# Kernel optimization log

Measured on AMD Instinct MI355X. Metric: run time of the kernel, lower is better.

## Reference

```python
import jax, jax.numpy as jnp
import numpy as np

N = 100000
E = 1600000
IN, HID, OUT = 128, 256, 64


def _glorot(key, fan_in, fan_out):
    s = 1.0 / np.sqrt(fan_in)
    return jax.random.uniform(key, (fan_in, fan_out), jnp.float32, -s, s)


def setup_inputs() -> dict:
    key = jax.random.key(0)
    ks = jax.random.split(key, 12)
    x = jax.random.normal(ks[0], (N, IN), jnp.float32)
    edge_index = jax.random.randint(ks[1], (2, E), 0, N, jnp.int64)
    dims = [(IN, HID), (HID, HID), (HID, OUT), (OUT, OUT)]
    inp = {"x": x, "edge_index": edge_index}
    for i, (fi, fo) in enumerate(dims, start=1):
        inp[f"Wl{i}"] = _glorot(ks[2 * i], fi, fo)        # aggregated-neighbor weight (lin_l)
        inp[f"Wr{i}"] = _glorot(ks[2 * i + 1], fi, fo)    # root/self weight (lin_r)
        inp[f"b{i}"] = jnp.zeros((fo,), jnp.float32)
    return inp


def _sage_conv(x, src, dst, Wl, Wr, b):
    # mean aggregation of source features into destination nodes
    msg_sum = jax.ops.segment_sum(x[src], dst, num_segments=N)           # [N, d_in]
    cnt = jax.ops.segment_sum(jnp.ones((src.shape[0],), x.dtype), dst, num_segments=N)
    mean = msg_sum / jnp.maximum(cnt, 1.0)[:, None]
    return mean @ Wl + x @ Wr + b


def reference(x, edge_index, Wl1, Wr1, b1, Wl2, Wr2, b2, Wl3, Wr3, b3, Wl4, Wr4, b4):
    src, dst = edge_index[0], edge_index[1]
    # conv1 = GraphSAGE(in, hid, num_layers=2): SAGEConv->ReLU->SAGEConv
    h = jax.nn.relu(_sage_conv(x, src, dst, Wl1, Wr1, b1))
    h = _sage_conv(h, src, dst, Wl2, Wr2, b2)
    # model-level ReLU between conv1 and conv2
    h = jax.nn.relu(h)
    # conv2 = GraphSAGE(hid, out, num_layers=2)
    h = jax.nn.relu(_sage_conv(h, src, dst, Wl3, Wr3, b3))
    h = _sage_conv(h, src, dst, Wl4, Wr4, b4)
    return jax.nn.log_softmax(h, axis=1)
```

## Files before the change

### kernel.cpp

```cpp
#include <hip/hip_runtime.h>
#include <cstdint>
#include <cstddef>


typedef short s16x8 __attribute__((ext_vector_type(8)));
typedef float f32x4 __attribute__((ext_vector_type(4)));
typedef float f32x2 __attribute__((ext_vector_type(2)));
typedef unsigned short u16;
typedef unsigned short u16x8 __attribute__((ext_vector_type(8)));
typedef unsigned char u8;
typedef unsigned char u8x8 __attribute__((ext_vector_type(8)));

#define EPB 8192
#define EPT 32
#define GCAP 6144

#if __has_builtin(__builtin_amdgcn_cvt_pk_f32_fp8) && __has_builtin(__builtin_amdgcn_cvt_pk_fp8_f32)
#define HWFP8 1
#else
#define HWFP8 0
#endif

__device__ __forceinline__ float b2f(u16 u) {
    union { unsigned int i; float f; } x; x.i = ((unsigned int)u) << 16; return x.f;
}
__device__ __forceinline__ u16 f2b(float f) {
    union { float f; unsigned int i; } x; x.f = f;
    unsigned int r = x.i + 0x7FFFu + ((x.i >> 16) & 1u);
    return (u16)(r >> 16);
}

#if !HWFP8
__device__ __forceinline__ u8 f2q_sw(float f) {
    union { float f; unsigned int i; } x; x.f = f;
    unsigned s = (x.i >> 24) & 0x80u;
    unsigned a = x.i & 0x7FFFFFFFu;
    a += 0x7FFFFu + ((a >> 20) & 1u);
    if (a < 0x3C800000u) return (u8)s;
    if (a > 0x43EFFFFFu) a = 0x43E00000u;
    unsigned e = (a >> 23) - 120u;
    unsigned m = (a >> 20) & 7u;
    return (u8)(s | (e << 3) | m);
}
__device__ __forceinline__ float q2f_sw(u8 u) {
    unsigned v = u & 0x7Fu;
    if (v == 0) return 0.f;
    union { unsigned int i; float f; } x;
    x.i = ((unsigned)(u & 0x80u) << 24) | (((v >> 3) + 120u) << 23) | ((v & 7u) << 20);
    return x.f;
}
#endif

__device__ __forceinline__ void dec8(u8x8 v, float* o) {
#if HWFP8
    union { u8x8 b; unsigned int d[2]; } u; u.b = v;
    f32x2 p;
    p = __builtin_amdgcn_cvt_pk_f32_fp8(u.d[0], false); o[0] = p[0]; o[1] = p[1];
    p = __builtin_amdgcn_cvt_pk_f32_fp8(u.d[0], true);  o[2] = p[0]; o[3] = p[1];
    p = __builtin_amdgcn_cvt_pk_f32_fp8(u.d[1], false); o[4] = p[0]; o[5] = p[1];
    p = __builtin_amdgcn_cvt_pk_f32_fp8(u.d[1], true);  o[6] = p[0]; o[7] = p[1];
#else
#pragma unroll
    for (int j = 0; j < 8; ++j) o[j] = q2f_sw(v[j]);
#endif
}
__device__ __forceinline__ u8x8 enc8(const float* f) {
#if HWFP8
    union { unsigned int d[2]; u8x8 b; } u;
    int d0 = __builtin_amdgcn_cvt_pk_fp8_f32(f[0], f[1], 0, false);
    d0 = __builtin_amdgcn_cvt_pk_fp8_f32(f[2], f[3], d0, true);
    int d1 = __builtin_amdgcn_cvt_pk_fp8_f32(f[4], f[5], 0, false);
    d1 = __builtin_amdgcn_cvt_pk_fp8_f32(f[6], f[7], d1, true);
    u.d[0] = (unsigned)d0; u.d[1] = (unsigned)d1;
    return u.b;
#else
    u8x8 q;
#pragma unroll
    for (int j = 0; j < 8; ++j) q[j] = f2q_sw(f[j]);
    return q;
#endif
}
__device__ __forceinline__ u8 enc1(float v) {
#if HWFP8
    return (u8)(__builtin_amdgcn_cvt_pk_fp8_f32(v, v, 0, false) & 0xFF);
#else
    return f2q_sw(v);
#endif
}


__global__ __launch_bounds__(256) void bucket_pass1(
    const int* __restrict__ src, const int* __restrict__ dst, int E,
    unsigned* __restrict__ gOffs, unsigned* __restrict__ staged, int nbkt)
{
    __shared__ unsigned offs[1025];
    __shared__ unsigned tsum[256];
    const int tid = threadIdx.x;
    const int e0 = blockIdx.x * EPB;

    for (int i = tid; i < nbkt; i += 256) offs[i] = 0u;
    __syncthreads();

    for (int t = 0; t < EPT; ++t) {
        int e = e0 + t * 256 + tid;
        if (e < E) atomicAdd(&offs[((unsigned)dst[e]) >> 7], 1u);
    }
    __syncthreads();

    unsigned c[4], sum = 0;
#pragma unroll
    for (int i = 0; i < 4; ++i) {
        int idx = tid * 4 + i;
        c[i] = sum;
        sum += (idx < nbkt) ? offs[idx] : 0u;
    }
    tsum[tid] = sum;
    __syncthreads();
    for (int off = 1; off < 256; off <<= 1) {
        unsigned v = (tid >= off) ? tsum[tid - off] : 0u;
        __syncthreads();
        tsum[tid] += v;
        __syncthreads();
    }
    unsigned base = (tid == 0) ? 0u : tsum[tid - 1];
    unsigned total = tsum[255];
#pragma unroll
    for (int i = 0; i < 4; ++i) {
        int idx = tid * 4 + i;
        if (idx < nbkt) offs[idx] = base + c[i];
    }
    if (tid == 0) offs[nbkt] = total;
    __syncthreads();

    for (int i = tid; i <= nbkt; i += 256)
        gOffs[(size_t)blockIdx.x * (nbkt + 1) + i] = offs[i];
    __syncthreads();

    for (int t = 0; t < EPT; ++t) {
        int e = e0 + t * 256 + tid;
        if (e < E) {
            unsigned d = (unsigned)dst[e];
            unsigned s = (unsigned)src[e];
            unsigned p = atomicAdd(&offs[d >> 7], 1u);
            staged[(size_t)e0 + p] = (s << 7) | (d & 127u);
        }
    }
}


__global__ void colsum_kernel(const unsigned* __restrict__ gOffs, int nblk, int nbkt,
                              unsigned* __restrict__ bktCnt) {
    int b = blockIdx.x * 256 + threadIdx.x;
    if (b >= nbkt) return;
    unsigned s = 0;
    for (int blk = 0; blk < nblk; ++blk) {
        const unsigned* row = gOffs + (size_t)blk * (nbkt + 1);
        s += row[b + 1] - row[b];
    }
    bktCnt[b] = s;
}


__global__ __launch_bounds__(1024) void scan_base(
    const unsigned* __restrict__ bktCnt, int nbkt, unsigned* __restrict__ bktBase)
{
    __shared__ unsigned lds[1024];
    int t = threadIdx.x;
    unsigned v = (t < nbkt) ? bktCnt[t] : 0u;
    lds[t] = v;
    __syncthreads();
    for (int off = 1; off < 1024; off <<= 1) {
        unsigned u = (t >= off) ? lds[t - off] : 0u;
        __syncthreads();
        lds[t] += u;
        __syncthreads();
    }
    if (t <= nbkt) bktBase[t] = lds[t] - v;
}


__global__ __launch_bounds__(256) void bucket_gather(
    const unsigned* __restrict__ gOffs, const unsigned* __restrict__ staged,
    const unsigned* __restrict__ bktBase, int nblk, int nbkt, int Nn, int E,
    int* __restrict__ ssrc, int* __restrict__ rp)
{
    __shared__ unsigned segS[256];
    __shared__ unsigned segBase[257];
    __shared__ unsigned tsum[256];
    __shared__ unsigned nodeCnt[128];
    __shared__ unsigned cursor[128];
    __shared__ unsigned ents[GCAP];
    const int tid = threadIdx.x;
    const int bkt = blockIdx.x;
    const int stride = nbkt + 1;

    unsigned len = 0;
    if (tid < nblk) {
        unsigned s = gOffs[(size_t)tid * stride + bkt];
        unsigned e = gOffs[(size_t)tid * stride + bkt + 1];
        segS[tid] = s;
        len = e - s;
    }
    tsum[tid] = len;
    __syncthreads();
    for (int off = 1; off < 256; off <<= 1) {
        unsigned u = (tid >= off) ? tsum[tid - off] : 0u;
        __syncthreads();
        tsum[tid] += u;
        __syncthreads();
    }
    segBase[tid] = tsum[tid] - len;
    if (tid == 255) segBase[256] = tsum[255];
    if (tid < 128) nodeCnt[tid] = 0u;
    __syncthreads();

    const unsigned total = segBase[nblk];
    const bool cached = (total <= (unsigned)GCAP);

    if (cached) {
        const int grp = tid >> 4, l16 = tid & 15;
        for (int sg = grp; sg < nblk; sg += 16) {
            unsigned b0 = segBase[sg];
            unsigned slen = segBase[sg + 1] - b0;
            unsigned s0 = segS[sg];
            for (unsigned j = l16; j < slen; j += 16)
                ents[b0 + j] = staged[(size_t)sg * EPB + s0 + j];
        }
        __syncthreads();
        for (unsigned p = tid; p < total; p += 256)
            atomicAdd(&nodeCnt[ents[p] & 127u], 1u);
    } else {
        for (unsigned p = tid; p < total; p += 256) {
            int lo = 0, hi = nblk;
            while (hi - lo > 1) {
                int mid = (lo + hi) >> 1;
                if (segBase[mid] <= p) lo = mid; else hi = mid;
            }
            unsigned ent = staged[(size_t)lo * EPB + segS[lo] + (p - segBase[lo])];
            atomicAdd(&nodeCnt[ent & 127u], 1u);
        }
    }
    __syncthreads();

    unsigned nc = (tid < 128) ? nodeCnt[tid] : 0u;
    tsum[tid] = nc;
    __syncthreads();
    for (int off = 1; off < 128; off <<= 1) {
        unsigned u = (tid >= off) ? tsum[tid - off] : 0u;
        __syncthreads();
        tsum[tid] += u;
        __syncthreads();
    }
    if (tid < 128) {
        unsigned off0 = tsum[tid] - nc;
        cursor[tid] = off0;
        int node = bkt * 128 + tid;
        if (node < Nn) rp[node] = (int)(bktBase[bkt] + off0);
    }
    if (bkt == 0 && tid == 0) rp[Nn] = E;
    __syncthreads();

    const unsigned gbase = bktBase[bkt];
    if (cached) {
        for (unsigned p = tid; p < total; p += 256) {
            unsigned ent = ents[p];
            unsigned pos = atomicAdd(&cursor[ent & 127u], 1u);
            ssrc[gbase + pos] = (int)(ent >> 7);
        }
    } else {
        for (unsigned p = tid; p < total; p += 256) {
            int lo = 0, hi = nblk;
            while (hi - lo > 1) {
                int mid = (lo + hi) >> 1;
                if (segBase[mid] <= p) lo = mid; else hi = mid;
            }
            unsigned ent = staged[(size_t)lo * EPB + segS[lo] + (p - segBase[lo])];
            unsigned pos = atomicAdd(&cursor[ent & 127u], 1u);
            ssrc[gbase + pos] = (int)(ent >> 7);
        }
    }
}


__device__ __forceinline__ void wtr(const float* W, int K, int Nout, u16* Wt,
                                    int rowOff, int idx) {
    int k = idx / Nout, n = idx - k * Nout;
    Wt[(size_t)(n + rowOff) * K + k] = f2b(W[idx]);
}

__global__ void prep_all(
    const float* __restrict__ x, u16* __restrict__ xb, u8* __restrict__ x8,
    long xchunks,
    const float* __restrict__ Wl1, const float* __restrict__ Wr1,
    const float* __restrict__ Wl2, const float* __restrict__ Wr2,
    const float* __restrict__ Wl3, const float* __restrict__ Wr3,
    const float* __restrict__ Wl4, const float* __restrict__ Wr4,
    const float* __restrict__ b3, const float* __restrict__ b4,
    u16* __restrict__ W1lt, u16* __restrict__ W1rt,
    u16* __restrict__ W2lt, u16* __restrict__ W2rt,
    u16* __restrict__ W3t,  u16* __restrict__ W4t,
    float* __restrict__ b3c, float* __restrict__ b4c)
{
    long gidx = (long)blockIdx.x * 256 + threadIdx.x;
    if (gidx < xchunks) {
        long i = gidx * 8;
        float4 a = *(const float4*)(x + i);
        float4 b = *(const float4*)(x + i + 4);
        float f[8] = {a.x, a.y, a.z, a.w, b.x, b.y, b.z, b.w};
        u16x8 v;
#pragma unroll
        for (int j = 0; j < 8; ++j) v[j] = f2b(f[j]);
        *(u16x8*)(xb + i) = v;
        *(u8x8*)(x8 + i) = enc8(f);
        return;
    }
    int idx = (int)(gidx - xchunks);
    if (idx < 32768) { wtr(Wl1, 128, 256, W1lt, 0, idx); return; }
    idx -= 32768;
    if (idx < 32768) { wtr(Wr1, 128, 256, W1rt, 0, idx); return; }
    idx -= 32768;
    if (idx < 65536) { wtr(Wl2, 256, 256, W2lt, 0, idx); return; }
    idx -= 65536;
    if (idx < 65536) { wtr(Wr2, 256, 256, W2rt, 0, idx); return; }
    idx -= 65536;
    if (idx < 16384) { wtr(Wl3, 256, 64, W3t, 0, idx); return; }
    idx -= 16384;
    if (idx < 16384) { wtr(Wr3, 256, 64, W3t, 64, idx); return; }
    idx -= 16384;
    if (idx < 4096)  { wtr(Wl4, 64, 64, W4t, 0, idx); return; }
    idx -= 4096;
    if (idx < 4096)  { wtr(Wr4, 64, 64, W4t, 64, idx); return; }
    idx -= 4096;
    if (idx < 128)   { b3c[idx] = (idx < 64) ? 0.f : b3[idx - 64]; return; }
    idx -= 128;
    if (idx < 128)   { b4c[idx] = (idx < 64) ? 0.f : b4[idx - 64]; return; }
}


template <int LPN, bool ADD, bool RELU, bool LSM>
__global__ __launch_bounds__(256) void agg_kernel(
    const u8* __restrict__ feat, int ldF,
    const u16* __restrict__ addB, int ldA, int offA,
    void* __restrict__ outp, int ldO,
    const int* __restrict__ rp, const int* __restrict__ ssrc, int Nn)
{
    constexpr int NPW = 64 / LPN;
    int lane = threadIdx.x & 63;
    int wid  = threadIdx.x >> 6;
    int sub  = lane / LPN;
    int sl   = lane % LPN;
    int n = (blockIdx.x * 4 + wid) * NPW + sub;
    if (n >= Nn) return;

    int s = rp[n], e = rp[n + 1];
    float acc[8] = {0.f, 0.f, 0.f, 0.f, 0.f, 0.f, 0.f, 0.f};
    const u8* fbase = feat + (size_t)sl * 8;

    float t[8];
    for (int k = s; k < e; k += 8) {
        int last = e - 1;
        int sc[8];
#pragma unroll
        for (int i = 0; i < 8; ++i) {
            int ki = k + i;
            sc[i] = ssrc[ki <= last ? ki : last];
        }
        u8x8 v[8];
#pragma unroll
        for (int i = 0; i < 8; ++i)
            v[i] = *(const u8x8*)(fbase + (size_t)sc[i] * ldF);
#pragma unroll
        for (int i = 0; i < 8; ++i) {
            if (k + i < e) {
                dec8(v[i], t);
#pragma unroll
                for (int j = 0; j < 8; ++j) acc[j] += t[j];
            }
        }
    }

    int cnt = e - s;
    float inv = 1.0f / (float)(cnt > 0 ? cnt : 1);
#pragma unroll
    for (int j = 0; j < 8; ++j) acc[j] *= inv;

    if constexpr (ADD) {
        u16x8 v = *(const u16x8*)(addB + (size_t)n * ldA + offA + (size_t)sl * 8);
#pragma unroll
        for (int j = 0; j < 8; ++j) acc[j] += b2f(v[j]);
    }
    if constexpr (RELU) {
#pragma unroll
        for (int j = 0; j < 8; ++j) acc[j] = fmaxf(acc[j], 0.f);
    }

    if constexpr (LSM) {
        float m = acc[0];
#pragma unroll
        for (int j = 1; j < 8; ++j) m = fmaxf(m, acc[j]);
#pragma unroll
        for (int off = 1; off < 8; off <<= 1) m = fmaxf(m, __shfl_xor(m, off));
        float ss = 0.f;
#pragma unroll
        for (int j = 0; j < 8; ++j) ss += expf(acc[j] - m);
#pragma unroll
        for (int off = 1; off < 8; off <<= 1) ss += __shfl_xor(ss, off);
        float lse = m + logf(ss);
        float* o = (float*)outp + (size_t)n * ldO + (size_t)sl * 8;
        *(float4*)o = make_float4(acc[0] - lse, acc[1] - lse, acc[2] - lse, acc[3] - lse);
        *(float4*)(o + 4) = make_float4(acc[4] - lse, acc[5] - lse, acc[6] - lse, acc[7] - lse);
    } else {
        u16x8 v;
#pragma unroll
        for (int j = 0; j < 8; ++j) v[j] = f2b(acc[j]);
        *(u16x8*)((u16*)outp + (size_t)n * ldO + (size_t)sl * 8) = v;
    }
}


template <bool DUAL, bool RELU>
__global__ __launch_bounds__(512, 4) void gemm_mfma(
    const u16* __restrict__ A1, const u16* __restrict__ Wt1, int K1,
    const u16* __restrict__ A2, const u16* __restrict__ Wt2, int K2,
    const float* __restrict__ bias,
    u16* __restrict__ outp, int ldOut, int M, int gxRow,
    u8* __restrict__ out8, int ld8, int n8max)
{
    __shared__ u16 sA[256][72];
    __shared__ u16 sW[128][72];

    int rowblk, colblk;
    if constexpr (DUAL) {
        int bid = blockIdx.x;
        rowblk = (bid >> 4) * 8 + (bid & 7);
        colblk = (bid >> 3) & 1;
        if (rowblk >= gxRow) return;
    } else {
        rowblk = blockIdx.x;
        colblk = 0;
    }
    const int row0 = rowblk * 256;
    const int nB   = colblk * 128;

    const int tid = threadIdx.x;
    const int lane = tid & 63, wid = tid >> 6;
    const int wr = wid >> 1, wc = wid & 1;
    const int r16 = lane & 15, khalf = lane >> 4;
    f32x4 acc[4][4] = {};

#pragma unroll 1
    for (int s = 0; s < (DUAL ? 2 : 1); ++s) {
        const u16* A  = (s == 0) ? A1 : A2;
        const u16* Wt = (s == 0) ? Wt1 : Wt2;
        const int  K  = (s == 0) ? K1 : K2;
        for (int k0 = 0; k0 < K; k0 += 64) {
#pragma unroll
            for (int it = 0; it < 4; ++it) {
                int idx = it * 512 + tid;
                int r = idx >> 3, kq = (idx & 7) * 8;
                int grow = row0 + r;
                s16x8 v = {};
                if (grow < M) v = *(const s16x8*)(A + (size_t)grow * K + k0 + kq);
                *(s16x8*)&sA[r][kq] = v;
            }
#pragma unroll
            for (int it = 0; it < 2; ++it) {
                int idx = it * 512 + tid;
                int r = idx >> 3, kq = (idx & 7) * 8;
                s16x8 v = *(const s16x8*)(Wt + (size_t)(nB + r) * K + k0 + kq);
                *(s16x8*)&sW[r][kq] = v;
            }
            __syncthreads();

#pragma unroll
            for (int ks = 0; ks < 2; ++ks) {
                const int kb = ks * 32 + khalf * 8;
                s16x8 af[4], bfr[4];
#pragma unroll
                for (int m = 0; m < 4; ++m)
                    af[m] = *(const s16x8*)&sA[wr * 64 + m * 16 + r16][kb];
#pragma unroll
                for (int nn = 0; nn < 4; ++nn)
                    bfr[nn] = *(const s16x8*)&sW[wc * 64 + nn * 16 + r16][kb];
#pragma unroll
                for (int m = 0; m < 4; ++m)
#pragma unroll
                    for (int nn = 0; nn < 4; ++nn)
                        acc[m][nn] = __builtin_amdgcn_mfma_f32_16x16x32_bf16(
                            af[m], bfr[nn], acc[m][nn], 0, 0, 0);
            }
            __syncthreads();
        }
    }

    float bv[4];
#pragma unroll
    for (int nn = 0; nn < 4; ++nn)
        bv[nn] = bias ? bias[nB + wc * 64 + nn * 16 + r16] : 0.f;
#pragma unroll
    for (int m = 0; m < 4; ++m) {
#pragma unroll
        for (int r = 0; r < 4; ++r) {
            int grow = row0 + wr * 64 + m * 16 + khalf * 4 + r;
            if (grow < M) {
#pragma unroll
                for (int nn = 0; nn < 4; ++nn) {
                    int col = nB + wc * 64 + nn * 16 + r16;
                    float v = acc[m][nn][r] + bv[nn];
                    if constexpr (RELU) v = fmaxf(v, 0.f);
                    outp[(size_t)grow * ldOut + col] = f2b(v);
                    if (out8 && col < n8max)
                        out8[(size_t)grow * ld8 + col] = enc1(v);
                }
            }
        }
    }
}


extern "C" void kernel_launch(void* const* d_in, const int* in_sizes, int n_in,
                              void* d_out, int out_size, void* d_ws, size_t ws_size,
                              hipStream_t stream)
{
    const float* x   = (const float*)d_in[0];
    const int*   ei  = (const int*)d_in[1];
    const float* Wl1 = (const float*)d_in[2];
    const float* Wr1 = (const float*)d_in[3];
    const float* b1  = (const float*)d_in[4];
    const float* Wl2 = (const float*)d_in[5];
    const float* Wr2 = (const float*)d_in[6];
    const float* b2  = (const float*)d_in[7];
    const float* Wl3 = (const float*)d_in[8];
    const float* Wr3 = (const float*)d_in[9];
    const float* b3  = (const float*)d_in[10];
    const float* Wl4 = (const float*)d_in[11];
    const float* Wr4 = (const float*)d_in[12];
    const float* b4  = (const float*)d_in[13];
    float* outp = (float*)d_out;

    const int N = in_sizes[0] / 128;
    const int E = in_sizes[1] / 2;
    const int* src = ei;
    const int* dst = ei + E;

    const int nbkt = (N + 127) >> 7;
    const int nblk = (E + EPB - 1) / EPB;

    char* w = (char*)d_ws;
    auto alloc = [&](size_t bytes) -> char* {
        char* p = w;
        w += (bytes + 255) & ~(size_t)255;
        return p;
    };
    int* ssrc = (int*)alloc((size_t)E * 4);
    int* rp   = (int*)alloc((size_t)(N + 1) * 4);
    unsigned* bktCnt  = (unsigned*)alloc((size_t)nbkt * 4);
    unsigned* bktBase = (unsigned*)alloc((size_t)(nbkt + 1) * 4);
    u16* mean1 = (u16*)alloc((size_t)N * 128 * 2);
    u16* h1    = (u16*)alloc((size_t)N * 256 * 2);
    u16* agg2b = (u16*)alloc((size_t)N * 256 * 2);
    u16* h2s   = (u16*)alloc((size_t)N * 256 * 2);
    u8* h1_8   = (u8*)alloc((size_t)N * 256);
    u8* t3_8   = (u8*)alloc((size_t)N * 64);
    u8* t4_8   = (u8*)alloc((size_t)N * 64);
    u16* W1lt = (u16*)alloc((size_t)256 * 128 * 2);
    u16* W1rt = (u16*)alloc((size_t)256 * 128 * 2);
    u16* W2lt = (u16*)alloc((size_t)256 * 256 * 2);
    u16* W2rt = (u16*)alloc((size_t)256 * 256 * 2);
    u16* W3t  = (u16*)alloc((size_t)128 * 256 * 2);
    u16* W4t  = (u16*)alloc((size_t)128 * 64 * 2);
    float* b3c = (float*)alloc(128 * 4);
    float* b4c = (float*)alloc(128 * 4);

    unsigned* staged = (unsigned*)h2s;
    unsigned* gOffs  = staged + (size_t)nblk * EPB;

    u16* xb   = h2s;
    u8*  x8   = (u8*)h2s + (size_t)N * 256;
    u16* h2   = h2s;
    u16* t3r3 = mean1;
    u16* h3   = h1;
    u16* t4r4 = h1 + (size_t)N * 64;

    dim3 blk(256);
    dim3 blkG(512);
    const int gx = (N + 255) / 256;
    const int gDual = ((gx + 7) / 8) * 16;

    bucket_pass1<<<nblk, blk, 0, stream>>>(src, dst, E, gOffs, staged, nbkt);
    colsum_kernel<<<(nbkt + 255) / 256, blk, 0, stream>>>(gOffs, nblk, nbkt, bktCnt);
    scan_base<<<1, 1024, 0, stream>>>(bktCnt, nbkt, bktBase);
    bucket_gather<<<nbkt, blk, 0, stream>>>(gOffs, staged, bktBase, nblk, nbkt, N, E,
                                            ssrc, rp);

    long xchunks = (long)N * 128 / 8;
    long ptot = xchunks + 237824;
    prep_all<<<(int)((ptot + 255) / 256), blk, 0, stream>>>(
        x, xb, x8, xchunks,
        Wl1, Wr1, Wl2, Wr2, Wl3, Wr3, Wl4, Wr4, b3, b4,
        W1lt, W1rt, W2lt, W2rt, W3t, W4t, b3c, b4c);

    agg_kernel<16, false, false, false><<<(N + 15) / 16, blk, 0, stream>>>(
        x8, 128, nullptr, 0, 0, mean1, 128, rp, ssrc, N);
    gemm_mfma<true, true><<<gDual, blkG, 0, stream>>>(
        mean1, W1lt, 128, xb, W1rt, 128, b1, h1, 256, N, gx, h1_8, 256, 256);

    agg_kernel<32, false, false, false><<<(N + 7) / 8, blk, 0, stream>>>(
        h1_8, 256, nullptr, 0, 0, agg2b, 256, rp, ssrc, N);
    gemm_mfma<true, true><<<gDual, blkG, 0, stream>>>(
        agg2b, W2lt, 256, h1, W2rt, 256, b2, h2, 256, N, gx, nullptr, 0, 0);

    gemm_mfma<false, false><<<gx, blkG, 0, stream>>>(
        h2, W3t, 256, nullptr, nullptr, 0, b3c, t3r3, 128, N, gx, t3_8, 64, 64);
    agg_kernel<8, true, true, false><<<(N + 31) / 32, blk, 0, stream>>>(
        t3_8, 64, t3r3, 128, 64, h3, 64, rp, ssrc, N);

    gemm_mfma<false, false><<<gx, blkG, 0, stream>>>(
        h3, W4t, 64, nullptr, nullptr, 0, b4c, t4r4, 128, N, gx, t4_8, 64, 64);
    agg_kernel<8, true, false, true><<<(N + 31) / 32, blk, 0, stream>>>(
        t4_8, 64, t4r4, 128, 64, outp, 64, rp, ssrc, N);
}
```

Baseline: 381.4 us.

## Load GEMM tiles directly into LDS with XOR-swizzled layout

Replaces the register-staged global-to-shared tile copies in the MFMA GEMM with direct global_load_lds transfers of 16 bytes per lane. The padded shared arrays become dense 64-wide rows, and an XOR swizzle on the 16-byte chunk index is applied on both the write and the read side to avoid bank conflicts. This aims to cut VGPR use and the extra LDS-write instructions, but rows past M are no longer zero-filled, so stale LDS data may enter the accumulators for out-of-range rows.

```diff
diff --git a/kernel.cpp b/kernel.cpp
--- a/kernel.cpp
+++ b/kernel.cpp
@@ -86,6 +86,13 @@
 #else
     return f2q_sw(v);
 #endif
+}
+
+__device__ __forceinline__ void gload16(const u16* gp, u16* lp) {
+    __builtin_amdgcn_global_load_lds(
+        (const __attribute__((address_space(1))) unsigned int*)gp,
+        (__attribute__((address_space(3))) unsigned int*)lp,
+        16, 0, 0);
 }
 
 
@@ -426,8 +433,8 @@
     u16* __restrict__ outp, int ldOut, int M, int gxRow,
     u8* __restrict__ out8, int ld8, int n8max)
 {
-    __shared__ u16 sA[256][72];
-    __shared__ u16 sW[128][72];
+    __shared__ u16 sA[256 * 64];
+    __shared__ u16 sW[128 * 64];
 
     int rowblk, colblk;
     if constexpr (DUAL) {
@@ -446,6 +453,10 @@
     const int lane = tid & 63, wid = tid >> 6;
     const int wr = wid >> 1, wc = wid & 1;
     const int r16 = lane & 15, khalf = lane >> 4;
+    const int lrow = lane >> 3;
+    const int lkel = (((lane & 7) ^ lrow) << 3);
+    const int rxor = (r16 & 7) << 4;
+
     f32x4 acc[4][4] = {};
 
 #pragma unroll 1
@@ -456,32 +467,33 @@
         for (int k0 = 0; k0 < K; k0 += 64) {
 #pragma unroll
             for (int it = 0; it < 4; ++it) {
-                int idx = it * 512 + tid;
-                int r = idx >> 3, kq = (idx & 7) * 8;
-                int grow = row0 + r;
-                s16x8 v = {};
-                if (grow < M) v = *(const s16x8*)(A + (size_t)grow * K + k0 + kq);
-                *(s16x8*)&sA[r][kq] = v;
+                int q = wid * 4 + it;
+                int grow = row0 + q * 8 + lrow;
+                if (grow < M)
+                    gload16(A + (size_t)grow * K + k0 + lkel, sA + q * 512);
             }
 #pragma unroll
             for (int it = 0; it < 2; ++it) {
-                int idx = it * 512 + tid;
-                int r = idx >> 3, kq = (idx & 7) * 8;
-                s16x8 v = *(const s16x8*)(Wt + (size_t)(nB + r) * K + k0 + kq);
-                *(s16x8*)&sW[r][kq] = v;
+                int q = wid * 2 + it;
+                int gr = nB + q * 8 + lrow;
+                gload16(Wt + (size_t)gr * K + k0 + lkel, sW + q * 512);
             }
             __syncthreads();
 
 #pragma unroll
             for (int ks = 0; ks < 2; ++ks) {
-                const int kb = ks * 32 + khalf * 8;
+                const int kb2 = (ks * 64 + khalf * 16) ^ rxor;
                 s16x8 af[4], bfr[4];
 #pragma unroll
-                for (int m = 0; m < 4; ++m)
-                    af[m] = *(const s16x8*)&sA[wr * 64 + m * 16 + r16][kb];
-#pragma unroll
-                for (int nn = 0; nn < 4; ++nn)
-                    bfr[nn] = *(const s16x8*)&sW[wc * 64 + nn * 16 + r16][kb];
+                for (int m = 0; m < 4; ++m) {
+                    int row = wr * 64 + m * 16 + r16;
+                    af[m] = *(const s16x8*)((const char*)sA + row * 128 + kb2);
+                }
+#pragma unroll
+                for (int nn = 0; nn < 4; ++nn) {
+                    int row = wc * 64 + nn * 16 + r16;
+                    bfr[nn] = *(const s16x8*)((const char*)sW + row * 128 + kb2);
+                }
 #pragma unroll
                 for (int m = 0; m < 4; ++m)
 #pragma unroll
```

Result: faster. 364.0 us (-4.6%).
